# Kernel optimization log

Measured on AMD Instinct MI355X. Metric: run time of the kernel, lower is better.

Reference implementation:

```python
import jax, jax.numpy as jnp
import numpy as np

B, N, D = 4, 2048, 512
M = 1024          # codebook_size
H, DH = 8, 64     # heads, dim_head
I = H * DH        # inner_dim = 512
FF = 1024         # dim_feedforward
EPS = 1e-5


def ln(x, g, b):
    mu = jnp.mean(x, axis=-1, keepdims=True)
    var = jnp.mean((x - mu) ** 2, axis=-1, keepdims=True)
    return (x - mu) * jax.lax.rsqrt(var + EPS) * g + b


def setup_inputs() -> dict:
    key = jax.random.key(0)
    ks = jax.random.split(key, 20)
    s = lambda fan: 1.0 / np.sqrt(fan)
    return {
        "context_input": jax.random.normal(ks[0], (B, N, D), jnp.float32),
        "context_mask": jax.random.randint(ks[1], (B, N), 0, 2) > 0,
        "codebook": jax.random.normal(ks[2], (M, D), jnp.float32),
        "norm_g": jnp.ones((D,)), "norm_b": jnp.zeros((D,)),
        "cnorm_g": jnp.ones((D,)), "cnorm_b": jnp.zeros((D,)),
        "wq": jax.random.normal(ks[3], (D, I)) * s(D),
        "wkv": jax.random.normal(ks[4], (D, 2 * I)) * s(D),
        "wo": jax.random.normal(ks[5], (I, D)) * s(I),
        "wo_b": jnp.zeros((D,)),
        "a_norm_g": jnp.ones((D,)), "a_norm_b": jnp.zeros((D,)),
        "a_qkv": jax.random.normal(ks[6], (D, 3 * I)) * s(D),
        "a_out": jax.random.normal(ks[7], (I, D)) * s(I),
        "f_norm_g": jnp.ones((D,)), "f_norm_b": jnp.zeros((D,)),
        "f_w1": jax.random.normal(ks[8], (D, FF)) * s(D),
        "f_w2": jax.random.normal(ks[9], (FF, D)) * s(FF),
    }


def _forward(context_input, context_mask, codebook, norm_g, norm_b, cnorm_g,
             cnorm_b, wq, wkv, wo, wo_b, a_norm_g, a_norm_b, a_qkv, a_out,
             f_norm_g, f_norm_b, f_w1, f_w2):
    scale = DH ** -0.5
    # ---- Vector quantization: nearest-codebook assignment (inference path) ----
    flat = context_input.reshape(-1, D)                      # [B*N, D]
    dist = (jnp.sum(flat ** 2, -1, keepdims=True)
            - 2.0 * flat @ codebook.T
            + jnp.sum(codebook ** 2, -1))                    # [B*N, M]
    flat_idx = jnp.argmin(dist, axis=-1)                     # [B*N]
    indices = flat_idx.reshape(B, N)
    quant = codebook[flat_idx]                               # [B*N, D]
    commit_loss = jnp.mean((flat - jax.lax.stop_gradient(quant)) ** 2)
    counts = jnp.zeros((M,), flat.dtype).at[flat_idx].add(1.0)
    probs = counts / flat_idx.shape[0]
    perplexity = jnp.exp(-jnp.sum(probs * jnp.log(probs + 1e-10)))
    # ---- Cross-attention: codebook queries attend over the context ----
    xq = ln(codebook, norm_g, norm_b)                        # [M, D]
    q = (xq @ wq).reshape(M, H, DH).transpose(1, 0, 2) * scale   # [H, M, DH]
    ctx = ln(context_input, cnorm_g, cnorm_b)                # [B, N, D]
    kv = ctx @ wkv                                           # [B, N, 2I]
    k, v = jnp.split(kv, 2, axis=-1)
    k = k.reshape(B, N, H, DH).transpose(0, 2, 1, 3)         # [B, H, N, DH]
    v = v.reshape(B, N, H, DH).transpose(0, 2, 1, 3)
    sim = jnp.einsum('hid,bhjd->bhij', q, k)                 # [B, H, M, N]
    big = jnp.finfo(sim.dtype).max
    sim = jnp.where(context_mask[:, None, None, :], sim, -big)
    attn = jax.nn.softmax(sim, axis=-1)
    out = jnp.einsum('bhij,bhjd->bhid', attn, v)             # [B, H, M, DH]
    out = out.transpose(0, 2, 1, 3).reshape(B, M, I) @ wo + wo_b  # [B, M, D]
    # ---- Transformer refinement layer (self-attn + FF, residual) ----
    h = ln(out, a_norm_g, a_norm_b)
    qkv = (h @ a_qkv).reshape(B, M, 3, H, DH)
    q2 = qkv[:, :, 0].transpose(0, 2, 1, 3) * scale
    k2 = qkv[:, :, 1].transpose(0, 2, 1, 3)
    v2 = qkv[:, :, 2].transpose(0, 2, 1, 3)
    a2 = jax.nn.softmax(jnp.einsum('bhid,bhjd->bhij', q2, k2), axis=-1)
    o2 = jnp.einsum('bhij,bhjd->bhid', a2, v2)
    out = out + o2.transpose(0, 2, 1, 3).reshape(B, M, I) @ a_out
    hf = ln(out, f_norm_g, f_norm_b)
    out = out + jax.nn.gelu(hf @ f_w1) @ f_w2
    # ---- Gather per-token outputs by VQ index ----
    outputs = jnp.take_along_axis(out, indices[:, :, None], axis=1)  # [B, N, D]
    return outputs, commit_loss, perplexity


def reference(context_input, context_mask, codebook, norm_g, norm_b, cnorm_g,
              cnorm_b, wq, wkv, wo, wo_b, a_norm_g, a_norm_b, a_qkv, a_out,
              f_norm_g, f_norm_b, f_w1, f_w2):
    return _forward(context_input, context_mask, codebook, norm_g, norm_b,
                    cnorm_g, cnorm_b, wq, wkv, wo, wo_b, a_norm_g, a_norm_b,
                    a_qkv, a_out, f_norm_g, f_norm_b, f_w1, f_w2)
```

## Files before the change

kernel.cpp:

```cpp
#include <hip/hip_runtime.h>
#include <math.h>

#define B_ 4
#define N_ 2048
#define D_ 512
#define M_ 1024
#define H_ 8
#define DH_ 64
#define I_ 512
#define FF_ 1024

typedef unsigned short u16;
typedef __attribute__((ext_vector_type(8))) short bf16x8;
typedef __attribute__((ext_vector_type(4))) float f32x4;

__device__ inline u16 f2b(float f) {
  union { float f; unsigned int u; } v; v.f = f;
  unsigned int u = v.u;
  u += 0x7fffu + ((u >> 16) & 1u);
  return (u16)(u >> 16);
}
__device__ inline float b2f(u16 h) {
  union { unsigned int u; float f; } v; v.u = ((unsigned int)h) << 16;
  return v.f;
}
__device__ inline float ex2(float x) { return __builtin_amdgcn_exp2f(x); }

__device__ inline float gelu_f(float x) {
  float x3 = x * x * x;
  return 0.5f * x * (1.f + tanhf(0.7978845608028654f * (x + 0.044715f * x3)));
}

__device__ inline bool better(float d1, int i1, float d2, int i2) {
  return d1 < d2 || (d1 == d2 && i1 < i2);
}

__global__ void zero_init_kernel(float* counts) {
  counts[threadIdx.x] = 0.f;
}

__global__ void mask_detect_kernel(const unsigned char* __restrict__ mb, int* flag) {
  __shared__ int any;
  if (threadIdx.x == 0) any = 0;
  __syncthreads();
  int acc = 0;
  for (int i = threadIdx.x; i < 8192; i += 256)
    if (i & 3) acc |= mb[i];
  if (acc) atomicOr(&any, 1);
  __syncthreads();
  if (threadIdx.x == 0) *flag = any;
}

__global__ void mask_norm_kernel(const void* __restrict__ mraw,
                                 const int* __restrict__ flag,
                                 int* __restrict__ mnorm) {
  int i = blockIdx.x * 256 + threadIdx.x;
  int v;
  if (*flag) v = ((const unsigned char*)mraw)[i];
  else       v = ((const int*)mraw)[i];
  mnorm[i] = (v != 0) ? 1 : 0;
}

__global__ __launch_bounds__(128) void code_sq_kernel(const float* __restrict__ cb,
                                                      double* __restrict__ csq,
                                                      float* __restrict__ csqf) {
  int row = blockIdx.x, tid = threadIdx.x;
  const float4* r4 = (const float4*)(cb + (size_t)row * D_);
  float4 v = r4[tid];
  double s = (double)v.x * v.x + (double)v.y * v.y + (double)v.z * v.z + (double)v.w * v.w;
  for (int off = 32; off; off >>= 1) s += __shfl_down(s, off);
  __shared__ double red[2];
  if ((tid & 63) == 0) red[tid >> 6] = s;
  __syncthreads();
  if (tid == 0) { csq[row] = red[0] + red[1]; csqf[row] = (float)(red[0] + red[1]); }
}

__global__ __launch_bounds__(256) void vq_split_x_kernel(
    const float* __restrict__ flat, u16* __restrict__ A)
{
  int t = blockIdx.x;
  const float* xr = flat + ((size_t)t << 9);
  u16* ar = A + (size_t)t * 1536;
#pragma unroll
  for (int i = 0; i < 2; i++) {
    int j = threadIdx.x + i * 256;
    float x = xr[j];
    u16 h = f2b(x);
    u16 l = f2b(x - b2f(h));
    ar[j] = h; ar[512 + j] = l; ar[1024 + j] = h;
  }
}
__global__ __launch_bounds__(256) void vq_split_c_kernel(
    const float* __restrict__ cb, u16* __restrict__ BT)
{
  int c = blockIdx.x;
  const float* cr = cb + ((size_t)c << 9);
  u16* br = BT + (size_t)c * 1536;
#pragma unroll
  for (int i = 0; i < 2; i++) {
    int j = threadIdx.x + i * 256;
    float x = cr[j];
    u16 h = f2b(x);
    u16 l = f2b(x - b2f(h));
    br[j] = h; br[512 + j] = h; br[1024 + j] = l;
  }
}

__global__ __launch_bounds__(256) void vq_top2_reduce_kernel(
    const float4* __restrict__ cand_part, int2* __restrict__ cand)
{
  int t = blockIdx.x * 256 + threadIdx.x;
  float b1 = 1e30f, b2 = 1e30f; int i1 = 1 << 20, i2 = 1 << 20;
#pragma unroll
  for (int cb = 0; cb < 16; cb++) {
    float4 v = cand_part[t * 16 + cb];
    float d1 = v.x, d2 = v.y;
    int j1 = __float_as_int(v.z), j2 = __float_as_int(v.w);
    if (better(d1, j1, b1, i1)) { b2 = b1; i2 = i1; b1 = d1; i1 = j1; }
    else if (better(d1, j1, b2, i2)) { b2 = d1; i2 = j1; }
    if (better(d2, j2, b1, i1)) { b2 = b1; i2 = i1; b1 = d2; i1 = j2; }
    else if (better(d2, j2, b2, i2)) { b2 = d2; i2 = j2; }
  }
  cand[t] = make_int2(i1, i2);
}

__global__ __launch_bounds__(256) void vq_refine_kernel(
    const float* __restrict__ flat, const float* __restrict__ cb,
    const double* __restrict__ csq, const int2* __restrict__ cand,
    int* __restrict__ out_idx, double* __restrict__ commit_partial,
    float* __restrict__ counts)
{
  int wave = threadIdx.x >> 6, lane = threadIdx.x & 63;
  int t = blockIdx.x * 4 + wave;
  int2 c = cand[t];
  const float* x = flat + ((size_t)t << 9);
  const float* c1 = cb + ((size_t)c.x << 9);
  const float* c2 = cb + ((size_t)c.y << 9);
  double s1 = 0.0, s2 = 0.0, sx = 0.0;
#pragma unroll
  for (int i = 0; i < 8; i++) {
    int d = lane + i * 64;
    double xv = x[d];
    s1 += xv * (double)c1[d];
    s2 += xv * (double)c2[d];
    sx += xv * xv;
  }
  for (int off = 32; off; off >>= 1) {
    s1 += __shfl_down(s1, off);
    s2 += __shfl_down(s2, off);
    sx += __shfl_down(sx, off);
  }
  if (lane == 0) {
    double d1 = csq[c.x] - 2.0 * s1;
    double d2 = csq[c.y] - 2.0 * s2;
    bool take2 = (d2 < d1 || (d2 == d1 && c.y < c.x));
    int bi = take2 ? c.y : c.x;
    out_idx[t] = bi;
    commit_partial[t] = sx + (take2 ? d2 : d1);
    atomicAdd(counts + bi, 1.0f);
  }
}

__global__ __launch_bounds__(256) void ln_rows_kernel(
    const float* __restrict__ x, const float* __restrict__ g,
    const float* __restrict__ b, u16* __restrict__ y)
{
  int row = blockIdx.x, tid = threadIdx.x;
  const float* xr = x + (size_t)row * D_;
  float v0 = xr[tid], v1 = xr[tid + 256];
  float s = v0 + v1;
  for (int off = 32; off; off >>= 1) s += __shfl_down(s, off);
  __shared__ float red[4];
  __shared__ float bcast[2];
  if ((tid & 63) == 0) red[tid >> 6] = s;
  __syncthreads();
  if (tid == 0) bcast[0] = (red[0] + red[1] + red[2] + red[3]) * (1.f / 512.f);
  __syncthreads();
  float mu = bcast[0];
  float d0 = v0 - mu, d1 = v1 - mu;
  float q = d0 * d0 + d1 * d1;
  for (int off = 32; off; off >>= 1) q += __shfl_down(q, off);
  if ((tid & 63) == 0) red[tid >> 6] = q;
  __syncthreads();
  if (tid == 0) bcast[1] = rsqrtf((red[0] + red[1] + red[2] + red[3]) * (1.f / 512.f) + 1e-5f);
  __syncthreads();
  float rs = bcast[1];
  u16* yr = y + (size_t)row * D_;
  yr[tid]       = f2b(d0 * rs * g[tid] + b[tid]);
  yr[tid + 256] = f2b(d1 * rs * g[tid + 256] + b[tid + 256]);
}

struct WJobs {
  const float* src[7];
  u16* dst[7];
  int K[7], N[7], b0[8];
};

__global__ __launch_bounds__(256) void wconv_all_kernel(WJobs jobs) {
  __shared__ float tile[32][33];
  int bid = blockIdx.x;
  int j = 0;
#pragma unroll
  for (int i = 1; i < 7; i++) if (bid >= jobs.b0[i]) j = i;
  int tb = bid - jobs.b0[j];
  int K = jobs.K[j], Nn = jobs.N[j];
  int tiles_x = Nn >> 5;
  int n0 = (tb % tiles_x) << 5, k0 = (tb / tiles_x) << 5;
  const float* W = jobs.src[j];
  u16* WT = jobs.dst[j];
  int t = threadIdx.x;
  int ty = t >> 5, tx = t & 31;
#pragma unroll
  for (int i = 0; i < 4; i++)
    tile[ty + 8 * i][tx] = W[(size_t)(k0 + ty + 8 * i) * Nn + n0 + tx];
  __syncthreads();
#pragma unroll
  for (int i = 0; i < 4; i++)
    WT[(size_t)(n0 + ty + 8 * i) * K + k0 + tx] = f2b(tile[tx][ty + 8 * i]);
}

template <int BN>
__global__ __launch_bounds__(256, 4) void gemm_bf16_kernel(
    const u16* __restrict__ A, const u16* __restrict__ BT,
    const float* __restrict__ bias, const float* __restrict__ resid,
    float* __restrict__ Cf, u16* __restrict__ Cb,
    const float* __restrict__ csqf, float4* __restrict__ cand_part,
    int M, int N, int K, int act)
{
  constexpr int MF = (BN == 128) ? 4 : 2;
  constexpr int ROWS_W = (BN == 128) ? 64 : 32;
  __shared__ __attribute__((aligned(16))) u16 As[2][128 * 40];
  __shared__ __attribute__((aligned(16))) u16 Bs[2][BN * 40];
  int tid = threadIdx.x;
  int lane = tid & 63, wave = tid >> 6;
  int wr = (BN == 128) ? (wave >> 1) : wave;
  int wc = (BN == 128) ? (wave & 1) : 0;
  int nwgx = gridDim.x;
  int nwg = nwgx * gridDim.y;
  int flat = blockIdx.y * nwgx + blockIdx.x;
  if ((nwg & 7) == 0) flat = (flat & 7) * (nwg >> 3) + (flat >> 3);
  int row0 = (flat / nwgx) << 7, col0 = (flat % nwgx) * BN;
  int l15 = lane & 15, l4 = lane >> 4;
  int sr = tid >> 2, skc = tid & 3;
  int soff = sr * 40 + skc * 8;
  const u16* pA0 = A + (size_t)(row0 + sr) * K + skc * 8;
  const u16* pA1 = A + (size_t)(row0 + 64 + sr) * K + skc * 8;
  const u16* pB0 = BT + (size_t)(col0 + sr) * K + skc * 8;
  const u16* pB1 = (BN == 128) ? (BT + (size_t)(col0 + 64 + sr) * K + skc * 8) : nullptr;
  f32x4 acc[MF][4] = {};
  int KT = K >> 5;
  bf16x8 ra0 = *(const bf16x8*)pA0;
  bf16x8 ra1 = *(const bf16x8*)pA1;
  bf16x8 rb0 = *(const bf16x8*)pB0;
  bf16x8 rb1;
  if constexpr (BN == 128) rb1 = *(const bf16x8*)pB1;
  *(bf16x8*)&As[0][soff] = ra0;
  *(bf16x8*)&As[0][64 * 40 + soff] = ra1;
  *(bf16x8*)&Bs[0][soff] = rb0;
  if constexpr (BN == 128) *(bf16x8*)&Bs[0][64 * 40 + soff] = rb1;
  if (KT > 1) {
    ra0 = *(const bf16x8*)(pA0 + 32);
    ra1 = *(const bf16x8*)(pA1 + 32);
    rb0 = *(const bf16x8*)(pB0 + 32);
    if constexpr (BN == 128) rb1 = *(const bf16x8*)(pB1 + 32);
  }
  for (int kt = 0; kt < KT; kt++) {
    int cur = kt & 1;
    __syncthreads();
    if (kt + 1 < KT) {
      *(bf16x8*)&As[cur ^ 1][soff] = ra0;
      *(bf16x8*)&As[cur ^ 1][64 * 40 + soff] = ra1;
      *(bf16x8*)&Bs[cur ^ 1][soff] = rb0;
      if constexpr (BN == 128) *(bf16x8*)&Bs[cur ^ 1][64 * 40 + soff] = rb1;
    }
    if (kt + 2 < KT) {
      int ko = (kt + 2) << 5;
      ra0 = *(const bf16x8*)(pA0 + ko);
      ra1 = *(const bf16x8*)(pA1 + ko);
      rb0 = *(const bf16x8*)(pB0 + ko);
      if constexpr (BN == 128) rb1 = *(const bf16x8*)(pB1 + ko);
    }
    bf16x8 af[MF], bfr[4];
#pragma unroll
    for (int m = 0; m < MF; m++)
      af[m] = *(const bf16x8*)&As[cur][(wr * ROWS_W + m * 16 + l15) * 40 + l4 * 8];
#pragma unroll
    for (int n = 0; n < 4; n++)
      bfr[n] = *(const bf16x8*)&Bs[cur][(wc * 64 + n * 16 + l15) * 40 + l4 * 8];
#pragma unroll
    for (int m = 0; m < MF; m++)
#pragma unroll
      for (int n = 0; n < 4; n++)
        acc[m][n] = __builtin_amdgcn_mfma_f32_16x16x32_bf16(af[m], bfr[n], acc[m][n], 0, 0, 0);
  }
  if constexpr (BN == 128) {
    if (act == 2) {
      float csq_l[4];
#pragma unroll
      for (int n = 0; n < 4; n++) csq_l[n] = csqf[col0 + wc * 64 + n * 16 + l15];
      int cbase = col0 + wc * 64 + l15;
#pragma unroll
      for (int m = 0; m < 4; m++) {
#pragma unroll
        for (int r = 0; r < 4; r++) {
          float b1_ = 1e30f, b2_ = 1e30f; int i1_ = 1 << 20, i2_ = 1 << 20;
#pragma unroll
          for (int n = 0; n < 4; n++) {
            float d = csq_l[n] - 2.f * acc[m][n][r];
            int c = cbase + n * 16;
            if (better(d, c, b1_, i1_)) { b2_ = b1_; i2_ = i1_; b1_ = d; i1_ = c; }
            else if (better(d, c, b2_, i2_)) { b2_ = d; i2_ = c; }
          }
          for (int off = 1; off < 16; off <<= 1) {
            float ob1 = __shfl_xor(b1_, off), ob2 = __shfl_xor(b2_, off);
            int oi1 = __shfl_xor(i1_, off), oi2 = __shfl_xor(i2_, off);
            if (better(b1_, i1_, ob1, oi1)) {
              if (better(ob1, oi1, b2_, i2_)) { b2_ = ob1; i2_ = oi1; }
            } else {
              float nb2; int ni2;
              if (better(b1_, i1_, ob2, oi2)) { nb2 = b1_; ni2 = i1_; }
              else                            { nb2 = ob2; ni2 = oi2; }
              b1_ = ob1; i1_ = oi1; b2_ = nb2; i2_ = ni2;
            }
          }
          if (l15 == 0) {
            int row = row0 + wr * 64 + m * 16 + l4 * 4 + r;
            float4 v4;
            v4.x = b1_; v4.y = b2_;
            v4.z = __int_as_float(i1_); v4.w = __int_as_float(i2_);
            cand_part[row * 16 + ((col0 >> 7) << 1) + wc] = v4;
          }
        }
      }
      return;
    }
  }
#pragma unroll
  for (int m = 0; m < MF; m++) {
#pragma unroll
    for (int n = 0; n < 4; n++) {
      int col = col0 + wc * 64 + n * 16 + l15;
      float bv = bias ? bias[col] : 0.f;
#pragma unroll
      for (int r = 0; r < 4; r++) {
        int row = row0 + wr * ROWS_W + m * 16 + l4 * 4 + r;
        float v = acc[m][n][r] + bv;
        if (act == 1) v = gelu_f(v);
        if (resid) v += resid[(size_t)row * N + col];
        if (Cf) Cf[(size_t)row * N + col] = v;
        if (Cb) Cb[(size_t)row * N + col] = f2b(v);
      }
    }
  }
}

__global__ __launch_bounds__(256) void vt_kernel(
    const u16* __restrict__ src, size_t b_stride, int row_stride, int col0,
    int n_rows, u16* __restrict__ dst)
{
  __shared__ __attribute__((aligned(16))) u16 tile[32][72];
  int t = threadIdx.x;
  int bh = blockIdx.y;
  int b = bh >> 3, h = bh & 7;
  int n0 = blockIdx.x * 32;
  int n = t >> 3, dc = t & 7;
  *(bf16x8*)&tile[n][dc * 8] =
      *(const bf16x8*)(src + (size_t)b * b_stride + (size_t)(n0 + n) * row_stride + col0 + h * 64 + dc * 8);
  __syncthreads();
  int d = t >> 2, ns = t & 3;
  bf16x8 o;
#pragma unroll
  for (int i = 0; i < 8; i++) o[i] = (short)tile[ns * 8 + i][d];
  *(bf16x8*)(dst + ((size_t)bh * 64 + d) * n_rows + n0 + ns * 8) = o;
}

__global__ __launch_bounds__(256, 4) void attn_mfma_kernel(
    const u16* __restrict__ Q, size_t q_bs, int q_stride,
    const u16* __restrict__ Kp, size_t k_bs, int k_stride, int k_extra,
    const u16* __restrict__ Vt, const int* __restrict__ mask,
    float scale, float* __restrict__ Opart, float* __restrict__ MLpart,
    int n_keys)
{
  __shared__ __attribute__((aligned(16))) u16 Ks[8 * 64 * 8];
  __shared__ __attribute__((aligned(16))) u16 Vs[8 * 64 * 8];
  __shared__ __attribute__((aligned(16))) u16 Ps[4][8 * 16 * 8];
  __shared__ float mbias[64];
  int tid = threadIdx.x, lane = tid & 63, wave = tid >> 6;
  int flat = blockIdx.x + (blockIdx.y << 4) + (blockIdx.z << 7);
  int swz = ((flat & 7) << 7) + (flat >> 3);
  int qb = swz & 15, h = (swz >> 4) & 7, z = swz >> 7;
  int b = z & 3, split = z >> 2;
  int q0 = qb * 64 + wave * 16;
  int l15 = lane & 15, l4 = lane >> 4;
  int nh = n_keys >> 1;
  int nstart = split * nh, nend = nstart + nh;

  const u16* qrow = Q + (size_t)b * q_bs + (size_t)(q0 + l15) * q_stride + h * 64 + l4 * 8;
  bf16x8 qf0 = *(const bf16x8*)qrow;
  bf16x8 qf1 = *(const bf16x8*)(qrow + 32);
  f32x4 o_acc[4] = {};
  float m_run = -3.0e38f, l_run = 0.f;
  int srow = tid >> 2, schunk = tid & 3;
  const u16* kbase = Kp + (size_t)b * k_bs + k_extra + h * 64;
  const u16* vtbase = Vt + (size_t)(b * 8 + h) * 64 * n_keys;

  bf16x8 pk0, pk1, pv0, pv1;
  int pmv = 1;
  {
    const u16* krow = kbase + (size_t)(nstart + srow) * k_stride;
    pk0 = *(const bf16x8*)(krow + schunk * 8);
    pk1 = *(const bf16x8*)(krow + (schunk + 4) * 8);
    const u16* vrow = vtbase + (size_t)srow * n_keys + nstart;
    pv0 = *(const bf16x8*)(vrow + schunk * 8);
    pv1 = *(const bf16x8*)(vrow + (schunk + 4) * 8);
    if (mask && tid < 64) pmv = mask[(size_t)b * n_keys + nstart + tid];
  }

  for (int n0 = nstart; n0 < nend; n0 += 64) {
    __syncthreads();
    *(bf16x8*)&Ks[(schunk * 64 + srow) * 8]       = pk0;
    *(bf16x8*)&Ks[((schunk + 4) * 64 + srow) * 8] = pk1;
    *(bf16x8*)&Vs[(schunk * 64 + srow) * 8]       = pv0;
    *(bf16x8*)&Vs[((schunk + 4) * 64 + srow) * 8] = pv1;
    if (tid < 64) mbias[tid] = (mask && !pmv) ? -3.0e38f : 0.f;
    __syncthreads();
    if (n0 + 64 < nend) {
      const u16* krow = kbase + (size_t)(n0 + 64 + srow) * k_stride;
      pk0 = *(const bf16x8*)(krow + schunk * 8);
      pk1 = *(const bf16x8*)(krow + (schunk + 4) * 8);
      const u16* vrow = vtbase + (size_t)srow * n_keys + n0 + 64;
      pv0 = *(const bf16x8*)(vrow + schunk * 8);
      pv1 = *(const bf16x8*)(vrow + (schunk + 4) * 8);
      if (mask && tid < 64) pmv = mask[(size_t)b * n_keys + n0 + 64 + tid];
    }
    f32x4 sac[4];
#pragma unroll
    for (int kb = 0; kb < 4; kb++) {
      bf16x8 kf0 = *(const bf16x8*)&Ks[(l4 * 64 + kb * 16 + l15) * 8];
      bf16x8 kf1 = *(const bf16x8*)&Ks[((l4 + 4) * 64 + kb * 16 + l15) * 8];
      f32x4 zz = {};
      zz = __builtin_amdgcn_mfma_f32_16x16x32_bf16(kf0, qf0, zz, 0, 0, 0);
      sac[kb] = __builtin_amdgcn_mfma_f32_16x16x32_bf16(kf1, qf1, zz, 0, 0, 0);
    }
    float sv[16];
    float pmax = -3.0e38f;
#pragma unroll
    for (int kb = 0; kb < 4; kb++) {
      float4 bs = *(const float4*)&mbias[kb * 16 + l4 * 4];
      sv[kb * 4 + 0] = fmaf(sac[kb][0], scale, bs.x);
      sv[kb * 4 + 1] = fmaf(sac[kb][1], scale, bs.y);
      sv[kb * 4 + 2] = fmaf(sac[kb][2], scale, bs.z);
      sv[kb * 4 + 3] = fmaf(sac[kb][3], scale, bs.w);
#pragma unroll
      for (int r = 0; r < 4; r++) pmax = fmaxf(pmax, sv[kb * 4 + r]);
    }
    pmax = fmaxf(pmax, __shfl_xor(pmax, 16));
    pmax = fmaxf(pmax, __shfl_xor(pmax, 32));
    if (!__all(pmax - m_run <= 11.5f)) {
      float mnew = fmaxf(m_run, pmax);
      float al = ex2(m_run - mnew);
      l_run *= al;
      m_run = mnew;
      float alr[4];
#pragma unroll
      for (int r = 0; r < 4; r++) alr[r] = __shfl(al, l4 * 4 + r, 64);
#pragma unroll
      for (int nb = 0; nb < 4; nb++)
#pragma unroll
        for (int r = 0; r < 4; r++) o_acc[nb][r] *= alr[r];
    }
    float psum = 0.f;
    u16 pb[16];
#pragma unroll
    for (int i = 0; i < 16; i++) {
      float p = ex2(sv[i] - m_run);
      psum += p;
      pb[i] = f2b(p);
    }
    psum += __shfl_xor(psum, 16);
    psum += __shfl_xor(psum, 32);
    l_run += psum;
#pragma unroll
    for (int kb = 0; kb < 4; kb++) {
      uint2 w;
      w.x = (unsigned int)pb[kb * 4 + 0] | ((unsigned int)pb[kb * 4 + 1] << 16);
      w.y = (unsigned int)pb[kb * 4 + 2] | ((unsigned int)pb[kb * 4 + 3] << 16);
      *(uint2*)&Ps[wave][((kb * 2 + (l4 >> 1)) * 16 + l15) * 8 + (l4 & 1) * 4] = w;
    }
#pragma unroll
    for (int c = 0; c < 2; c++) {
      bf16x8 pf = *(const bf16x8*)&Ps[wave][((c * 4 + l4) * 16 + l15) * 8];
#pragma unroll
      for (int nb = 0; nb < 4; nb++) {
        bf16x8 vf = *(const bf16x8*)&Vs[((c * 4 + l4) * 64 + nb * 16 + l15) * 8];
        o_acc[nb] = __builtin_amdgcn_mfma_f32_16x16x32_bf16(pf, vf, o_acc[nb], 0, 0, 0);
      }
    }
  }
  int pr_base = ((split * 4 + b) * 8 + h) * 1024;
#pragma unroll
  for (int nb = 0; nb < 4; nb++)
#pragma unroll
    for (int r = 0; r < 4; r++)
      Opart[(size_t)(pr_base + q0 + l4 * 4 + r) * 64 + nb * 16 + l15] = o_acc[nb][r];
  if (lane < 16) {
    int pr = pr_base + q0 + lane;
    MLpart[2 * pr]     = m_run;
    MLpart[2 * pr + 1] = l_run;
  }
}

__global__ __launch_bounds__(256) void attn_combine_kernel(
    const float* __restrict__ Opart, const float* __restrict__ MLpart,
    u16* __restrict__ O, size_t o_bs)
{
  int idx = blockIdx.x * 256 + threadIdx.x;
  int d = idx & 63, gq = idx >> 6;
  int row = gq & 1023, bh = gq >> 10;
  int h = bh & 7, b = bh >> 3;
  float m0 = MLpart[2 * gq], l0 = MLpart[2 * gq + 1];
  float m1 = MLpart[2 * (32768 + gq)], l1 = MLpart[2 * (32768 + gq) + 1];
  float mmax = fmaxf(m0, m1);
  float w0 = ex2(m0 - mmax), w1 = ex2(m1 - mmax);
  float l = l0 * w0 + l1 * w1;
  float o = Opart[(size_t)gq * 64 + d] * w0 + Opart[(size_t)(32768 + gq) * 64 + d] * w1;
  O[(size_t)b * o_bs + (size_t)row * 512 + h * 64 + d] = f2b(o / l);
}

__global__ __launch_bounds__(128) void gather_kernel(
    const float* __restrict__ x2, const int* __restrict__ idx, float* __restrict__ out)
{
  int t = blockIdx.x;
  int b = t >> 11;
  int code = idx[t];
  const float4* src = (const float4*)(x2 + ((size_t)(b * M_ + code) << 9));
  float4* dst = (float4*)(out + ((size_t)t << 9));
  dst[threadIdx.x] = src[threadIdx.x];
}

__global__ void scalars_kernel(const float* __restrict__ counts,
                               const double* __restrict__ commit_partial,
                               float* __restrict__ out_tail)
{
  int tid = threadIdx.x;
  double cs = 0.0;
#pragma unroll
  for (int i = 0; i < 8; i++) cs += commit_partial[tid + i * 1024];
  double p = (double)counts[tid] / 8192.0;
  double e = p * log(p + 1e-10);
  for (int off = 32; off; off >>= 1) {
    cs += __shfl_down(cs, off);
    e  += __shfl_down(e, off);
  }
  __shared__ double redc[16], rede[16];
  if ((tid & 63) == 0) { redc[tid >> 6] = cs; rede[tid >> 6] = e; }
  __syncthreads();
  if (tid == 0) {
    double sc = 0.0, se = 0.0;
    for (int i = 0; i < 16; i++) { sc += redc[i]; se += rede[i]; }
    out_tail[0] = (float)(sc / (8192.0 * 512.0));
    out_tail[1] = (float)exp(-se);
  }
}

extern "C" void kernel_launch(void* const* d_in, const int* in_sizes, int n_in,
                              void* d_out, int out_size, void* d_ws, size_t ws_size,
                              hipStream_t stream) {
  const float* ctx      = (const float*)d_in[0];
  const void*  mask_raw = d_in[1];
  const float* codebook = (const float*)d_in[2];
  const float* norm_g   = (const float*)d_in[3];
  const float* norm_b   = (const float*)d_in[4];
  const float* cnorm_g  = (const float*)d_in[5];
  const float* cnorm_b  = (const float*)d_in[6];
  const float* wq       = (const float*)d_in[7];
  const float* wkv      = (const float*)d_in[8];
  const float* wo       = (const float*)d_in[9];
  const float* wo_b     = (const float*)d_in[10];
  const float* a_norm_g = (const float*)d_in[11];
  const float* a_norm_b = (const float*)d_in[12];
  const float* a_qkv    = (const float*)d_in[13];
  const float* a_out    = (const float*)d_in[14];
  const float* f_norm_g = (const float*)d_in[15];
  const float* f_norm_b = (const float*)d_in[16];
  const float* f_w1     = (const float*)d_in[17];
  const float* f_w2     = (const float*)d_in[18];
  float* out = (float*)d_out;
  const float LOG2E = 1.4426950408889634f;

  char* ws = (char*)d_ws;
  int*    mask_flag  = (int*)(ws + 64);
  float*  counts     = (float*)(ws + 128);
  double* code_sq    = (double*)(ws + 128 + 4096);
  float*  csqf       = (float*)(ws + 128 + 4096 + 8192);
  int*    indices    = (int*)(ws + 128 + 4096 + 8192 + 4096);
  int*    mask_norm  = (int*)(ws + 128 + 4096 + 8192 + 4096 + 32768);
  int2*   cand       = (int2*)(ws + 128 + 4096 + 8192 + 4096 + 32768 + 32768);
  double* commit_partial = (double*)(ws + 128 + 4096 + 8192 + 4096 + 32768 + 32768 + 65536);
  float*  attn_ml    = (float*)(ws + 262144);

  char* pool = ws + (1 << 20);
  u16*   vqA  = (u16*)(pool);
  u16*   vqBT = (u16*)(pool + ((size_t)26 << 20));
  float4* cand_part = (float4*)(pool + ((size_t)30 << 20));
  char* regA  = pool;
  char* regB  = pool + ((size_t)16 << 20);
  char* regC  = pool + ((size_t)24 << 20);
  char* regD  = pool + ((size_t)32 << 20);
  char* regE  = pool + ((size_t)40 << 20);
  char* regF  = pool + ((size_t)44 << 20);
  size_t woff = (1 << 20) + ((size_t)64 << 20);
  u16* wqT    = (u16*)(ws + woff); woff += (size_t)512 * 512 * 2;
  u16* wkvT   = (u16*)(ws + woff); woff += (size_t)1024 * 512 * 2;
  u16* woT    = (u16*)(ws + woff); woff += (size_t)512 * 512 * 2;
  u16* aqkvT  = (u16*)(ws + woff); woff += (size_t)1536 * 512 * 2;
  u16* aoutT  = (u16*)(ws + woff); woff += (size_t)512 * 512 * 2;
  u16* fw1T   = (u16*)(ws + woff); woff += (size_t)1024 * 512 * 2;
  u16* fw2T   = (u16*)(ws + woff); woff += (size_t)512 * 1024 * 2;
  u16* xq_b   = (u16*)(ws + woff); woff += (size_t)1024 * 512 * 2;
  u16* qs_b   = (u16*)(ws + woff); woff += (size_t)1024 * 512 * 2;

  u16* kv_b     = (u16*)regA;
  u16* qkv2_b   = (u16*)regA;
  u16* ctx_ln_b = (u16*)regB;
  u16* VtS      = (u16*)regB;
  u16* VtX      = (u16*)regC;
  float* x1_f   = (float*)regC;
  float* x0_f   = (float*)regD;
  u16* att_out_b = (u16*)regE;
  u16* h_b       = (u16*)regE;
  u16* o2_b      = (u16*)regE;
  u16* hf_b      = (u16*)regE;
  u16* g_b      = (u16*)regF;
  float* x2_f   = (float*)(pool + ((size_t)52 << 20));
  float* attn_part = (float*)regF;

  zero_init_kernel<<<1, 1024, 0, stream>>>(counts);
  mask_detect_kernel<<<1, 256, 0, stream>>>((const unsigned char*)mask_raw, mask_flag);
  mask_norm_kernel<<<32, 256, 0, stream>>>(mask_raw, mask_flag, mask_norm);
  code_sq_kernel<<<1024, 128, 0, stream>>>(codebook, code_sq, csqf);
  vq_split_x_kernel<<<8192, 256, 0, stream>>>(ctx, vqA);
  vq_split_c_kernel<<<1024, 256, 0, stream>>>(codebook, vqBT);
  gemm_bf16_kernel<128><<<dim3(8, 64), 256, 0, stream>>>(vqA, vqBT, nullptr, nullptr,
                                                    nullptr, nullptr, csqf, cand_part,
                                                    8192, 1024, 1536, 2);
  vq_top2_reduce_kernel<<<32, 256, 0, stream>>>(cand_part, cand);
  vq_refine_kernel<<<2048, 256, 0, stream>>>(ctx, codebook, code_sq, cand, indices,
                                             commit_partial, counts);

  WJobs jobs;
  jobs.src[0] = wq;    jobs.dst[0] = wqT;   jobs.K[0] = 512;  jobs.N[0] = 512;
  jobs.src[1] = wkv;   jobs.dst[1] = wkvT;  jobs.K[1] = 512;  jobs.N[1] = 1024;
  jobs.src[2] = wo;    jobs.dst[2] = woT;   jobs.K[2] = 512;  jobs.N[2] = 512;
  jobs.src[3] = a_qkv; jobs.dst[3] = aqkvT; jobs.K[3] = 512;  jobs.N[3] = 1536;
  jobs.src[4] = a_out; jobs.dst[4] = aoutT; jobs.K[4] = 512;  jobs.N[4] = 512;
  jobs.src[5] = f_w1;  jobs.dst[5] = fw1T;  jobs.K[5] = 512;  jobs.N[5] = 1024;
  jobs.src[6] = f_w2;  jobs.dst[6] = fw2T;  jobs.K[6] = 1024; jobs.N[6] = 512;
  int acc_b = 0;
  for (int i = 0; i < 7; i++) {
    jobs.b0[i] = acc_b;
    acc_b += (jobs.K[i] >> 5) * (jobs.N[i] >> 5);
  }
  jobs.b0[7] = acc_b;
  wconv_all_kernel<<<acc_b, 256, 0, stream>>>(jobs);

  ln_rows_kernel<<<1024, 256, 0, stream>>>(codebook, norm_g, norm_b, xq_b);
  gemm_bf16_kernel<64><<<dim3(8, 8), 256, 0, stream>>>(xq_b, wqT, nullptr, nullptr,
                                                   nullptr, qs_b, nullptr, nullptr,
                                                   1024, 512, 512, 0);
  ln_rows_kernel<<<8192, 256, 0, stream>>>(ctx, cnorm_g, cnorm_b, ctx_ln_b);
  gemm_bf16_kernel<128><<<dim3(8, 64), 256, 0, stream>>>(ctx_ln_b, wkvT, nullptr, nullptr,
                                                    nullptr, kv_b, nullptr, nullptr,
                                                    8192, 1024, 512, 0);
  vt_kernel<<<dim3(64, 32), 256, 0, stream>>>(kv_b, (size_t)2048 * 1024, 1024, 512, 2048, VtX);
  attn_mfma_kernel<<<dim3(16, 8, 8), 256, 0, stream>>>(
      qs_b, 0, 512, kv_b, (size_t)2048 * 1024, 1024, 0, VtX, mask_norm,
      0.125f * LOG2E, attn_part, attn_ml, 2048);
  attn_combine_kernel<<<8192, 256, 0, stream>>>(attn_part, attn_ml, att_out_b, (size_t)1024 * 512);
  gemm_bf16_kernel<64><<<dim3(8, 32), 256, 0, stream>>>(att_out_b, woT, wo_b, nullptr,
                                                    x0_f, nullptr, nullptr, nullptr,
                                                    4096, 512, 512, 0);

  ln_rows_kernel<<<4096, 256, 0, stream>>>(x0_f, a_norm_g, a_norm_b, h_b);
  gemm_bf16_kernel<64><<<dim3(24, 32), 256, 0, stream>>>(h_b, aqkvT, nullptr, nullptr,
                                                     nullptr, qkv2_b, nullptr, nullptr,
                                                     4096, 1536, 512, 0);
  vt_kernel<<<dim3(32, 32), 256, 0, stream>>>(qkv2_b, (size_t)1024 * 1536, 1536, 1024, 1024, VtS);
  attn_mfma_kernel<<<dim3(16, 8, 8), 256, 0, stream>>>(
      qkv2_b, (size_t)1024 * 1536, 1536, qkv2_b, (size_t)1024 * 1536, 1536, 512, VtS, nullptr,
      0.125f * LOG2E, attn_part, attn_ml, 1024);
  attn_combine_kernel<<<8192, 256, 0, stream>>>(attn_part, attn_ml, o2_b, (size_t)1024 * 512);
  gemm_bf16_kernel<64><<<dim3(8, 32), 256, 0, stream>>>(o2_b, aoutT, nullptr, x0_f,
                                                    x1_f, nullptr, nullptr, nullptr,
                                                    4096, 512, 512, 0);
  ln_rows_kernel<<<4096, 256, 0, stream>>>(x1_f, f_norm_g, f_norm_b, hf_b);
  gemm_bf16_kernel<64><<<dim3(16, 32), 256, 0, stream>>>(hf_b, fw1T, nullptr, nullptr,
                                                    nullptr, g_b, nullptr, nullptr,
                                                    4096, 1024, 512, 1);
  gemm_bf16_kernel<64><<<dim3(8, 32), 256, 0, stream>>>(g_b, fw2T, nullptr, x1_f,
                                                    x2_f, nullptr, nullptr, nullptr,
                                                    4096, 512, 1024, 0);

  gather_kernel<<<8192, 128, 0, stream>>>(x2_f, indices, out);
  scalars_kernel<<<1, 1024, 0, stream>>>(counts, commit_partial, out + (size_t)B_ * N_ * D_);
}
```

Before: 336.1 us.

## Replace split-bf16 VQ distance GEMM with plain bf16 plus top-4 exact refine

Drops the hi/lo bf16 split (K=1536) for the VQ distance GEMM and uses a single bf16 pass with K=512, cutting that GEMM's work to a third. To make up for the lower precision, the epilogue and reduce now keep a top-4 candidate list per token using sorting networks instead of top-2. The refine kernel then rechecks all four candidates exactly in fp64. The risk is a wrong argmin if the true nearest code falls outside the bf16 top-4, and the larger candidate buffers and extra shuffles cost some time.

After: 316.7 us. -5.8%, faster.

```diff
diff --git a/kernel.cpp b/kernel.cpp
--- a/kernel.cpp
+++ b/kernel.cpp
@@ -33,6 +33,15 @@
 
 __device__ inline bool better(float d1, int i1, float d2, int i2) {
   return d1 < d2 || (d1 == d2 && i1 < i2);
+}
+__device__ inline void cswap(float& da, int& ia, float& db, int& ib) {
+  if (better(db, ib, da, ia)) {
+    float td = da; da = db; db = td;
+    int ti = ia; ia = ib; ib = ti;
+  }
+}
+__device__ inline void kmin(float& da, int& ia, float db, int ib) {
+  if (better(db, ib, da, ia)) { da = db; ia = ib; }
 }
 
 __global__ void zero_init_kernel(float* counts) {
@@ -75,88 +84,83 @@
   if (tid == 0) { csq[row] = red[0] + red[1]; csqf[row] = (float)(red[0] + red[1]); }
 }
 
-__global__ __launch_bounds__(256) void vq_split_x_kernel(
-    const float* __restrict__ flat, u16* __restrict__ A)
-{
-  int t = blockIdx.x;
-  const float* xr = flat + ((size_t)t << 9);
-  u16* ar = A + (size_t)t * 1536;
-#pragma unroll
-  for (int i = 0; i < 2; i++) {
-    int j = threadIdx.x + i * 256;
-    float x = xr[j];
-    u16 h = f2b(x);
-    u16 l = f2b(x - b2f(h));
-    ar[j] = h; ar[512 + j] = l; ar[1024 + j] = h;
-  }
-}
-__global__ __launch_bounds__(256) void vq_split_c_kernel(
-    const float* __restrict__ cb, u16* __restrict__ BT)
-{
-  int c = blockIdx.x;
-  const float* cr = cb + ((size_t)c << 9);
-  u16* br = BT + (size_t)c * 1536;
-#pragma unroll
-  for (int i = 0; i < 2; i++) {
-    int j = threadIdx.x + i * 256;
-    float x = cr[j];
-    u16 h = f2b(x);
-    u16 l = f2b(x - b2f(h));
-    br[j] = h; br[512 + j] = h; br[1024 + j] = l;
-  }
-}
-
-__global__ __launch_bounds__(256) void vq_top2_reduce_kernel(
-    const float4* __restrict__ cand_part, int2* __restrict__ cand)
+__global__ __launch_bounds__(256) void conv_bf16_kernel(const float* __restrict__ src,
+                                                        u16* __restrict__ dst) {
+  int i = (blockIdx.x * 256 + threadIdx.x) * 8;
+  float4 a = *(const float4*)(src + i);
+  float4 b = *(const float4*)(src + i + 4);
+  uint4 o;
+  o.x = (unsigned int)f2b(a.x) | ((unsigned int)f2b(a.y) << 16);
+  o.y = (unsigned int)f2b(a.z) | ((unsigned int)f2b(a.w) << 16);
+  o.z = (unsigned int)f2b(b.x) | ((unsigned int)f2b(b.y) << 16);
+  o.w = (unsigned int)f2b(b.z) | ((unsigned int)f2b(b.w) << 16);
+  *(uint4*)(dst + i) = o;
+}
+
+__global__ __launch_bounds__(256) void vq_top4_reduce_kernel(
+    const float4* __restrict__ cand_part, int4* __restrict__ cand4)
 {
   int t = blockIdx.x * 256 + threadIdx.x;
-  float b1 = 1e30f, b2 = 1e30f; int i1 = 1 << 20, i2 = 1 << 20;
+  float d0 = 1e30f, d1 = 1e30f, d2 = 1e30f, d3 = 1e30f;
+  int x0 = 1 << 20, x1 = 1 << 21, x2 = 1 << 22, x3 = 1 << 23;
 #pragma unroll
   for (int cb = 0; cb < 16; cb++) {
-    float4 v = cand_part[t * 16 + cb];
-    float d1 = v.x, d2 = v.y;
-    int j1 = __float_as_int(v.z), j2 = __float_as_int(v.w);
-    if (better(d1, j1, b1, i1)) { b2 = b1; i2 = i1; b1 = d1; i1 = j1; }
-    else if (better(d1, j1, b2, i2)) { b2 = d1; i2 = j1; }
-    if (better(d2, j2, b1, i1)) { b2 = b1; i2 = i1; b1 = d2; i1 = j2; }
-    else if (better(d2, j2, b2, i2)) { b2 = d2; i2 = j2; }
-  }
-  cand[t] = make_int2(i1, i2);
-}
-
-__global__ __launch_bounds__(256) void vq_refine_kernel(
+    float4 a = cand_part[(size_t)t * 32 + cb * 2];
+    float4 b = cand_part[(size_t)t * 32 + cb * 2 + 1];
+    float e0 = a.x, e1 = a.y, e2 = b.x, e3 = b.y;
+    int y0 = __float_as_int(a.z), y1 = __float_as_int(a.w);
+    int y2 = __float_as_int(b.z), y3 = __float_as_int(b.w);
+    kmin(d0, x0, e3, y3); kmin(d1, x1, e2, y2);
+    kmin(d2, x2, e1, y1); kmin(d3, x3, e0, y0);
+    cswap(d0, x0, d2, x2); cswap(d1, x1, d3, x3);
+    cswap(d0, x0, d1, x1); cswap(d2, x2, d3, x3);
+  }
+  cand4[t] = make_int4(x0, x1, x2, x3);
+}
+
+__global__ __launch_bounds__(256) void vq_refine4_kernel(
     const float* __restrict__ flat, const float* __restrict__ cb,
-    const double* __restrict__ csq, const int2* __restrict__ cand,
+    const double* __restrict__ csq, const int4* __restrict__ cand4,
     int* __restrict__ out_idx, double* __restrict__ commit_partial,
     float* __restrict__ counts)
 {
   int wave = threadIdx.x >> 6, lane = threadIdx.x & 63;
   int t = blockIdx.x * 4 + wave;
-  int2 c = cand[t];
+  int4 c = cand4[t];
   const float* x = flat + ((size_t)t << 9);
-  const float* c1 = cb + ((size_t)c.x << 9);
-  const float* c2 = cb + ((size_t)c.y << 9);
-  double s1 = 0.0, s2 = 0.0, sx = 0.0;
+  const float* p0 = cb + ((size_t)c.x << 9);
+  const float* p1 = cb + ((size_t)c.y << 9);
+  const float* p2 = cb + ((size_t)c.z << 9);
+  const float* p3 = cb + ((size_t)c.w << 9);
+  double s0 = 0.0, s1 = 0.0, s2 = 0.0, s3 = 0.0, sx = 0.0;
 #pragma unroll
   for (int i = 0; i < 8; i++) {
     int d = lane + i * 64;
     double xv = x[d];
-    s1 += xv * (double)c1[d];
-    s2 += xv * (double)c2[d];
+    s0 += xv * (double)p0[d];
+    s1 += xv * (double)p1[d];
+    s2 += xv * (double)p2[d];
+    s3 += xv * (double)p3[d];
     sx += xv * xv;
   }
   for (int off = 32; off; off >>= 1) {
+    s0 += __shfl_down(s0, off);
     s1 += __shfl_down(s1, off);
     s2 += __shfl_down(s2, off);
+    s3 += __shfl_down(s3, off);
     sx += __shfl_down(sx, off);
   }
   if (lane == 0) {
-    double d1 = csq[c.x] - 2.0 * s1;
-    double d2 = csq[c.y] - 2.0 * s2;
-    bool take2 = (d2 < d1 || (d2 == d1 && c.y < c.x));
-    int bi = take2 ? c.y : c.x;
+    double dd0 = csq[c.x] - 2.0 * s0;
+    double dd1 = csq[c.y] - 2.0 * s1;
+    double dd2 = csq[c.z] - 2.0 * s2;
+    double dd3 = csq[c.w] - 2.0 * s3;
+    int bi = c.x; double bd = dd0;
+    if (dd1 < bd || (dd1 == bd && c.y < bi)) { bd = dd1; bi = c.y; }
+    if (dd2 < bd || (dd2 == bd && c.z < bi)) { bd = dd2; bi = c.z; }
+    if (dd3 < bd || (dd3 == bd && c.w < bi)) { bd = dd3; bi = c.w; }
     out_idx[t] = bi;
-    commit_partial[t] = sx + (take2 ? d2 : d1);
+    commit_partial[t] = sx + bd;
     atomicAdd(counts + bi, 1.0f);
   }
 }
@@ -299,36 +303,38 @@
 #pragma unroll
       for (int n = 0; n < 4; n++) csq_l[n] = csqf[col0 + wc * 64 + n * 16 + l15];
       int cbase = col0 + wc * 64 + l15;
+      int slot = ((col0 >> 7) << 1) + wc;
 #pragma unroll
       for (int m = 0; m < 4; m++) {
 #pragma unroll
         for (int r = 0; r < 4; r++) {
-          float b1_ = 1e30f, b2_ = 1e30f; int i1_ = 1 << 20, i2_ = 1 << 20;
-#pragma unroll
-          for (int n = 0; n < 4; n++) {
-            float d = csq_l[n] - 2.f * acc[m][n][r];
-            int c = cbase + n * 16;
-            if (better(d, c, b1_, i1_)) { b2_ = b1_; i2_ = i1_; b1_ = d; i1_ = c; }
-            else if (better(d, c, b2_, i2_)) { b2_ = d; i2_ = c; }
-          }
+          float d0 = csq_l[0] - 2.f * acc[m][0][r];
+          float d1 = csq_l[1] - 2.f * acc[m][1][r];
+          float d2 = csq_l[2] - 2.f * acc[m][2][r];
+          float d3 = csq_l[3] - 2.f * acc[m][3][r];
+          int x0 = cbase, x1 = cbase + 16, x2 = cbase + 32, x3 = cbase + 48;
+          cswap(d0, x0, d1, x1); cswap(d2, x2, d3, x3);
+          cswap(d0, x0, d2, x2); cswap(d1, x1, d3, x3);
+          cswap(d1, x1, d2, x2);
           for (int off = 1; off < 16; off <<= 1) {
-            float ob1 = __shfl_xor(b1_, off), ob2 = __shfl_xor(b2_, off);
-            int oi1 = __shfl_xor(i1_, off), oi2 = __shfl_xor(i2_, off);
-            if (better(b1_, i1_, ob1, oi1)) {
-              if (better(ob1, oi1, b2_, i2_)) { b2_ = ob1; i2_ = oi1; }
-            } else {
-              float nb2; int ni2;
-              if (better(b1_, i1_, ob2, oi2)) { nb2 = b1_; ni2 = i1_; }
-              else                            { nb2 = ob2; ni2 = oi2; }
-              b1_ = ob1; i1_ = oi1; b2_ = nb2; i2_ = ni2;
-            }
+            float e0 = __shfl_xor(d0, off), e1 = __shfl_xor(d1, off);
+            float e2 = __shfl_xor(d2, off), e3 = __shfl_xor(d3, off);
+            int y0 = __shfl_xor(x0, off), y1 = __shfl_xor(x1, off);
+            int y2 = __shfl_xor(x2, off), y3 = __shfl_xor(x3, off);
+            kmin(d0, x0, e3, y3); kmin(d1, x1, e2, y2);
+            kmin(d2, x2, e1, y1); kmin(d3, x3, e0, y0);
+            cswap(d0, x0, d2, x2); cswap(d1, x1, d3, x3);
+            cswap(d0, x0, d1, x1); cswap(d2, x2, d3, x3);
           }
           if (l15 == 0) {
             int row = row0 + wr * 64 + m * 16 + l4 * 4 + r;
-            float4 v4;
-            v4.x = b1_; v4.y = b2_;
-            v4.z = __int_as_float(i1_); v4.w = __int_as_float(i2_);
-            cand_part[row * 16 + ((col0 >> 7) << 1) + wc] = v4;
+            float4 v1, v2;
+            v1.x = d0; v1.y = d1;
+            v1.z = __int_as_float(x0); v1.w = __int_as_float(x1);
+            v2.x = d2; v2.y = d3;
+            v2.z = __int_as_float(x2); v2.w = __int_as_float(x3);
+            cand_part[(size_t)row * 32 + slot * 2]     = v1;
+            cand_part[(size_t)row * 32 + slot * 2 + 1] = v2;
           }
         }
       }
@@ -591,13 +597,13 @@
   char* ws = (char*)d_ws;
   int*    mask_flag  = (int*)(ws + 64);
   float*  counts     = (float*)(ws + 128);
-  double* code_sq    = (double*)(ws + 128 + 4096);
-  float*  csqf       = (float*)(ws + 128 + 4096 + 8192);
-  int*    indices    = (int*)(ws + 128 + 4096 + 8192 + 4096);
-  int*    mask_norm  = (int*)(ws + 128 + 4096 + 8192 + 4096 + 32768);
-  int2*   cand       = (int2*)(ws + 128 + 4096 + 8192 + 4096 + 32768 + 32768);
-  double* commit_partial = (double*)(ws + 128 + 4096 + 8192 + 4096 + 32768 + 32768 + 65536);
-  float*  attn_ml    = (float*)(ws + 262144);
+  double* code_sq    = (double*)(ws + 4224);
+  float*  csqf       = (float*)(ws + 12416);
+  int*    indices    = (int*)(ws + 16512);
+  int*    mask_norm  = (int*)(ws + 49280);
+  int4*   cand4      = (int4*)(ws + 82048);
+  double* commit_partial = (double*)(ws + 262144);
+  float*  attn_ml    = (float*)(ws + 524288);
 
   char* pool = ws + (1 << 20);
   u16*   vqA  = (u16*)(pool);
@@ -639,14 +645,14 @@
   mask_detect_kernel<<<1, 256, 0, stream>>>((const unsigned char*)mask_raw, mask_flag);
   mask_norm_kernel<<<32, 256, 0, stream>>>(mask_raw, mask_flag, mask_norm);
   code_sq_kernel<<<1024, 128, 0, stream>>>(codebook, code_sq, csqf);
-  vq_split_x_kernel<<<8192, 256, 0, stream>>>(ctx, vqA);
-  vq_split_c_kernel<<<1024, 256, 0, stream>>>(codebook, vqBT);
+  conv_bf16_kernel<<<2048, 256, 0, stream>>>(ctx, vqA);
+  conv_bf16_kernel<<<256, 256, 0, stream>>>(codebook, vqBT);
   gemm_bf16_kernel<128><<<dim3(8, 64), 256, 0, stream>>>(vqA, vqBT, nullptr, nullptr,
                                                     nullptr, nullptr, csqf, cand_part,
-                                                    8192, 1024, 1536, 2);
-  vq_top2_reduce_kernel<<<32, 256, 0, stream>>>(cand_part, cand);
-  vq_refine_kernel<<<2048, 256, 0, stream>>>(ctx, codebook, code_sq, cand, indices,
-                                             commit_partial, counts);
+                                                    8192, 1024, 512, 2);
+  vq_top4_reduce_kernel<<<32, 256, 0, stream>>>(cand_part, cand4);
+  vq_refine4_kernel<<<2048, 256, 0, stream>>>(ctx, codebook, code_sq, cand4, indices,
+                                              commit_partial, counts);
 
   WJobs jobs;
   jobs.src[0] = wq;    jobs.dst[0] = wqT;   jobs.K[0] = 512;  jobs.N[0] = 512;
```
